# Performance work log

Hardware: AMD Instinct MI355X
Metric: run time of the kernel (lower is better)

## Reference

```python
import jax, jax.numpy as jnp
import numpy as np

NUM_USERS = 50000
NUM_ITEMS = 50000
N_NODES = NUM_USERS + NUM_ITEMS
DIM_FEAT = 256
HID = 128
EMB = 128
K = 3
N_EDGES = 1_600_000


def setup_inputs() -> dict:
    key = jax.random.key(0)
    ks = jax.random.split(key, 16)

    def xavier(k, shape):
        fan_in, fan_out = shape[-2], shape[-1]
        std = float(np.sqrt(2.0 / (fan_in + fan_out)))
        return jax.random.normal(k, shape, dtype=jnp.float32) * std

    return {
        "feat": jax.random.normal(ks[0], (NUM_ITEMS, DIM_FEAT), dtype=jnp.float32),
        "node_emb": jax.random.normal(ks[1], (N_NODES, EMB), dtype=jnp.float32),
        "src": jax.random.randint(ks[2], (N_EDGES,), 0, N_NODES, dtype=jnp.int32),
        "dst": jax.random.randint(ks[3], (N_EDGES,), 0, N_NODES, dtype=jnp.int32),
        "user_feat_emb": xavier(ks[4], (NUM_USERS, HID)),
        "trans_w": xavier(ks[5], (DIM_FEAT, HID)),
        "trans_b": jnp.zeros((HID,), dtype=jnp.float32),
        # layer 0: hidden->hidden; layers 1,2: emb->emb. hidden==emb so stack.
        "ws": xavier(ks[6], (K, HID, HID)),
        "des_w": xavier(ks[7], (K, HID, EMB)),
        "des_b": jnp.zeros((K, EMB), dtype=jnp.float32),
        # concat=True: outs[i] takes [h | u] of width hidden+emb
        "out_w": xavier(ks[8], (K, HID + EMB, EMB)),
        "out_b": jnp.zeros((K, EMB), dtype=jnp.float32),
    }


def reference(feat, node_emb, src, dst, user_feat_emb,
              trans_w, trans_b, ws, des_w, des_b, out_w, out_b):
    # feat = trans(feat); concat user embeddings; L2-normalize rows
    x = feat @ trans_w + trans_b                      # [num_items, HID]
    x = jnp.concatenate([user_feat_emb, x], axis=0)   # [N, HID]
    norm = jnp.linalg.norm(x, axis=1, keepdims=True)
    x = x / jnp.maximum(norm, 1e-12)

    lrelu = jax.nn.leaky_relu  # slope 0.01, matches F.leaky_relu default
    for i in range(K):
        # g.func(x, W): sparse adjacency aggregation (sum over in-edges) then dense W
        agg = jax.ops.segment_sum(x[src], dst, num_segments=N_NODES)  # [N, HID]
        h = lrelu(agg @ ws[i])                                        # [N, HID]
        u = lrelu(h @ des_w[i] + des_b[i] + node_emb)                 # [N, EMB]
        x = lrelu(jnp.concatenate([h, u], axis=1) @ out_w[i] + out_b[i])
    return x, user_feat_emb
```

## Files before the change

kernel.cpp:

```cpp
#include <hip/hip_runtime.h>

#define NN 100000
#define NU 50000
#define NI 50000
#define NE 1600000
#define NSLICE 2
#define SLICEW 50000

#define HSLICE 4
#define HCHUNK 64
#define HSW 25600
#define HEPC (NE/HCHUNK)

#define PREP_TW 14
#define PREP_CONV 6250
#define PREP_NORM 12500

typedef unsigned short u16;
typedef unsigned int u32;

typedef __attribute__((ext_vector_type(8))) short s16x8;
typedef __attribute__((ext_vector_type(4))) float f32x4;
typedef __attribute__((ext_vector_type(4))) unsigned short us4;

__device__ __forceinline__ float bf2f(u16 u){
  union { u32 i; float f; } v; v.i = ((u32)u) << 16; return v.f;
}
__device__ __forceinline__ u16 f2bf(float f){
  union { float f; u32 i; } v; v.f = f;
  u32 u = v.i;
  return (u16)((u + 0x7FFFu + ((u >> 16) & 1u)) >> 16);
}
__device__ __forceinline__ u32 pack2(float lo, float hi){
  return (u32)f2bf(lo) | ((u32)f2bf(hi) << 16);
}
__device__ __forceinline__ float lrelu(float x){ return x > 0.f ? x : 0.01f * x; }
__device__ __forceinline__ float san(float v){
  union { float f; u32 i; } u; u.f = v;
  return ((u.i & 0x7F800000u) == 0x7F800000u) ? 0.f : v;
}

__global__ __launch_bounds__(256) void prep(
    const float* __restrict__ trans_w, const float* __restrict__ wsw,
    const float* __restrict__ desw, const float* __restrict__ outw,
    u16* __restrict__ Ttw, u16* __restrict__ Tw, u16* __restrict__ Td, u16* __restrict__ To,
    const float* __restrict__ nemb, u16* __restrict__ nembB,
    const float* __restrict__ ufe, u16* __restrict__ X)
{
  __shared__ u16 L[128][136];
  int b = blockIdx.x, t = threadIdx.x;

  if (b < PREP_TW){
    const float* src; u16* dst; int stride;
    if (b < 2)      { src = trans_w + b*16384;        dst = Ttw + b*128;          stride = 256; }
    else if (b < 5) { int i = b-2; src = wsw  + i*16384; dst = Tw + i*16384;      stride = 128; }
    else if (b < 8) { int i = b-5; src = desw + i*16384; dst = Td + i*16384;      stride = 128; }
    else            { int i = (b-8)>>1, h = (b-8)&1;
                      src = outw + i*32768 + h*16384;    dst = To + i*32768 + h*128; stride = 256; }
    #pragma unroll
    for (int p = 0; p < 8; p++){
      int fi = (p*256 + t)*8;
      int r = fi >> 7, c = fi & 127;
      f32x4 v0 = *(const f32x4*)(src + r*128 + c);
      f32x4 v1 = *(const f32x4*)(src + r*128 + c + 4);
      L[c+0][r] = f2bf(san(v0.x)); L[c+1][r] = f2bf(san(v0.y));
      L[c+2][r] = f2bf(san(v0.z)); L[c+3][r] = f2bf(san(v0.w));
      L[c+4][r] = f2bf(san(v1.x)); L[c+5][r] = f2bf(san(v1.y));
      L[c+6][r] = f2bf(san(v1.z)); L[c+7][r] = f2bf(san(v1.w));
    }
    __syncthreads();
    #pragma unroll
    for (int p = 0; p < 8; p++){
      int fi = (p*256 + t)*8;
      int n = fi >> 7, k = fi & 127;
      us4 o0, o1;
      o0.x = L[n][k+0]; o0.y = L[n][k+1]; o0.z = L[n][k+2]; o0.w = L[n][k+3];
      o1.x = L[n][k+4]; o1.y = L[n][k+5]; o1.z = L[n][k+6]; o1.w = L[n][k+7];
      *(us4*)(dst + (size_t)n*stride + k)     = o0;
      *(us4*)(dst + (size_t)n*stride + k + 4) = o1;
    }
  } else if (b < PREP_TW + PREP_CONV){
    int i = (b - PREP_TW)*256 + t;
    size_t off = (size_t)i * 8;
    f32x4 v0 = *(const f32x4*)(nemb + off);
    f32x4 v1 = *(const f32x4*)(nemb + off + 4);
    us4 o0, o1;
    o0.x = f2bf(san(v0.x)); o0.y = f2bf(san(v0.y)); o0.z = f2bf(san(v0.z)); o0.w = f2bf(san(v0.w));
    o1.x = f2bf(san(v1.x)); o1.y = f2bf(san(v1.y)); o1.z = f2bf(san(v1.z)); o1.w = f2bf(san(v1.w));
    *(us4*)(nembB + off)     = o0;
    *(us4*)(nembB + off + 4) = o1;
  } else {
    int gid = (b - PREP_TW - PREP_CONV)*256 + t;
    int row = gid >> 6, lane = gid & 63;
    float2 v = *(const float2*)(ufe + (size_t)row*128 + lane*2);
    float a = san(v.x), bb = san(v.y);
    float ss = a*a + bb*bb;
    #pragma unroll
    for (int off = 32; off; off >>= 1) ss += __shfl_xor(ss, off, 64);
    float inv = 1.0f / fmaxf(sqrtf(ss), 1e-12f);
    *(u32*)(X + (size_t)row*128 + lane*2) = pack2(a*inv, bb*inv);
  }
}

__global__ __launch_bounds__(256, 4) void trans_items(
    const float* __restrict__ feat, const u16* __restrict__ Ttw,
    const float* __restrict__ tb, u16* __restrict__ X)
{
  __shared__ u16 Af[64][136];
  __shared__ float rowss[64][8];
  __shared__ float rnorm[64];

  int t = threadIdx.x;
  int r0 = blockIdx.x * 64;
  int w = t >> 6, lane = t & 63;
  int l15 = lane & 15, q = lane >> 4;
  int m0 = (w & 1) * 64, n0 = (w >> 1) * 32;

  f32x4 acc[4][2];
  #pragma unroll
  for (int mi = 0; mi < 4; mi++)
    #pragma unroll
    for (int ni = 0; ni < 2; ni++){ acc[mi][ni].x = 0.f; acc[mi][ni].y = 0.f; acc[mi][ni].z = 0.f; acc[mi][ni].w = 0.f; }

  for (int half = 0; half < 2; half++){
    __syncthreads();
    #pragma unroll
    for (int p = 0; p < 4; p++){
      int fi = (p*256 + t)*8;
      int r = fi >> 7, c = fi & 127;
      int row = r0 + r;
      us4 o0 = {0,0,0,0}, o1 = {0,0,0,0};
      if (row < NI){
        f32x4 v0 = *(const f32x4*)(feat + (size_t)row*256 + half*128 + c);
        f32x4 v1 = *(const f32x4*)(feat + (size_t)row*256 + half*128 + c + 4);
        o0.x = f2bf(san(v0.x)); o0.y = f2bf(san(v0.y)); o0.z = f2bf(san(v0.z)); o0.w = f2bf(san(v0.w));
        o1.x = f2bf(san(v1.x)); o1.y = f2bf(san(v1.y)); o1.z = f2bf(san(v1.z)); o1.w = f2bf(san(v1.w));
      }
      *(us4*)&Af[r][c]     = o0;
      *(us4*)&Af[r][c + 4] = o1;
    }
    __syncthreads();
    #pragma unroll
    for (int kc = 0; kc < 128; kc += 32){
      s16x8 afr[4], bfr[2];
      #pragma unroll
      for (int mi = 0; mi < 4; mi++)
        afr[mi] = *(const s16x8*)(Ttw + (size_t)(m0 + 16*mi + l15)*256 + half*128 + kc + 8*q);
      #pragma unroll
      for (int ni = 0; ni < 2; ni++) bfr[ni] = *(const s16x8*)&Af[n0 + 16*ni + l15][kc + 8*q];
      #pragma unroll
      for (int mi = 0; mi < 4; mi++)
        #pragma unroll
        for (int ni = 0; ni < 2; ni++)
          acc[mi][ni] = __builtin_amdgcn_mfma_f32_16x16x32_bf16(afr[mi], bfr[ni], acc[mi][ni], 0, 0, 0);
    }
  }

  float bias[4][4];
  #pragma unroll
  for (int mi = 0; mi < 4; mi++){
    int c0 = m0 + 16*mi + 4*q;
    f32x4 bv = *(const f32x4*)(tb + c0);
    bias[mi][0] = san(bv.x); bias[mi][1] = san(bv.y); bias[mi][2] = san(bv.z); bias[mi][3] = san(bv.w);
  }
  #pragma unroll
  for (int ni = 0; ni < 2; ni++){
    float ss = 0.f;
    #pragma unroll
    for (int mi = 0; mi < 4; mi++){
      float v0 = acc[mi][ni].x + bias[mi][0];
      float v1 = acc[mi][ni].y + bias[mi][1];
      float v2 = acc[mi][ni].z + bias[mi][2];
      float v3 = acc[mi][ni].w + bias[mi][3];
      ss += v0*v0 + v1*v1 + v2*v2 + v3*v3;
    }
    rowss[n0 + 16*ni + l15][(w & 1)*4 + q] = ss;
  }
  __syncthreads();
  if (t < 64){
    float s = 0.f;
    #pragma unroll
    for (int j = 0; j < 8; j++) s += rowss[t][j];
    rnorm[t] = 1.0f / fmaxf(sqrtf(s), 1e-12f);
  }
  __syncthreads();
  #pragma unroll
  for (int mi = 0; mi < 4; mi++){
    int c0 = m0 + 16*mi + 4*q;
    #pragma unroll
    for (int ni = 0; ni < 2; ni++){
      int r = n0 + 16*ni + l15;
      int row = r0 + r;
      if (row < NI){
        float inv = rnorm[r];
        us4 o;
        o.x = f2bf((acc[mi][ni].x + bias[mi][0]) * inv);
        o.y = f2bf((acc[mi][ni].y + bias[mi][1]) * inv);
        o.z = f2bf((acc[mi][ni].z + bias[mi][2]) * inv);
        o.w = f2bf((acc[mi][ni].w + bias[mi][3]) * inv);
        *(us4*)(X + (size_t)(NU + row)*128 + c0) = o;
      }
    }
  }
}

__global__ __launch_bounds__(1024) void hist_lds(
    const int* __restrict__ dst, u32* __restrict__ countsC)
{
  __shared__ u32 cnt[HSW];
  int b = blockIdx.x;
  int s = b / HCHUNK, c = b % HCHUNK;
  int t = threadIdx.x;
  for (int i = t; i < HSW; i += 1024) cnt[i] = 0;
  __syncthreads();
  int lo = s * HSW;
  int hi = min(lo + HSW, NN);
  int e0 = c * HEPC, e1 = e0 + HEPC;
  for (int e = e0 + t*4; e < e1; e += 4096){
    int4 d4 = *(const int4*)(dst + e);
    int d0 = min(max(d4.x, 0), NN-1);
    int d1 = min(max(d4.y, 0), NN-1);
    int d2 = min(max(d4.z, 0), NN-1);
    int d3 = min(max(d4.w, 0), NN-1);
    if (d0 >= lo && d0 < hi) atomicAdd(&cnt[d0 - lo], 1u);
    if (d1 >= lo && d1 < hi) atomicAdd(&cnt[d1 - lo], 1u);
    if (d2 >= lo && d2 < hi) atomicAdd(&cnt[d2 - lo], 1u);
    if (d3 >= lo && d3 < hi) atomicAdd(&cnt[d3 - lo], 1u);
  }
  __syncthreads();
  u32* outp = countsC + (size_t)c*NN + lo;
  int w = hi - lo;
  for (int i = t; i < w; i += 1024) outp[i] = cnt[i];
}

__global__ __launch_bounds__(256) void reduce_counts(
    const u32* __restrict__ countsC, int* __restrict__ counts)
{
  int v = blockIdx.x*256 + threadIdx.x;
  if (v < NN){
    u32 sum = 0;
    #pragma unroll
    for (int c = 0; c < HCHUNK; c++) sum += countsC[(size_t)c*NN + v];
    counts[v] = (int)sum;
  }
}

__global__ __launch_bounds__(1024) void scan_p1(
    const int* __restrict__ counts, int* __restrict__ row_ptr, int* __restrict__ bsum)
{
  __shared__ int wsum[16];
  __shared__ int woff[16];
  int t = threadIdx.x;
  int lane = t & 63, wid = t >> 6;
  int idx = blockIdx.x*4096 + t*4;
  int4 v = {0,0,0,0};
  if (idx < NN) v = *(const int4*)(counts + idx);
  int s4 = v.x + v.y + v.z + v.w;
  int s = s4;
  #pragma unroll
  for (int off = 1; off < 64; off <<= 1){
    int u = __shfl_up(s, off, 64);
    if (lane >= off) s += u;
  }
  if (lane == 63) wsum[wid] = s;
  __syncthreads();
  if (t < 16){
    int ws = wsum[t];
    int wscan = ws;
    #pragma unroll
    for (int off = 1; off < 16; off <<= 1){
      int u = __shfl_up(wscan, off, 64);
      if (t >= off) wscan += u;
    }
    woff[t] = wscan - ws;
    if (t == 15) bsum[blockIdx.x] = wscan;
  }
  __syncthreads();
  if (idx < NN){
    int e0 = woff[wid] + (s - s4);
    int4 o;
    o.x = e0; o.y = e0 + v.x; o.z = o.y + v.y; o.w = o.z + v.z;
    *(int4*)(row_ptr + idx) = o;
  }
}

__global__ __launch_bounds__(64) void scan_p2(int* __restrict__ bsum, int nb)
{
  int t = threadIdx.x;
  int v = (t < nb) ? bsum[t] : 0;
  int s = v;
  #pragma unroll
  for (int off = 1; off < 64; off <<= 1){
    int u = __shfl_up(s, off, 64);
    if (t >= off) s += u;
  }
  if (t < nb) bsum[t] = s - v;
}

__global__ __launch_bounds__(1024) void scan_p3(
    int* __restrict__ row_ptr, const int* __restrict__ bsum)
{
  int c = bsum[blockIdx.x];
  if (c == 0) return;
  int idx = blockIdx.x*4096 + threadIdx.x*4;
  if (idx < NN){
    int4 o = *(int4*)(row_ptr + idx);
    o.x += c; o.y += c; o.z += c; o.w += c;
    *(int4*)(row_ptr + idx) = o;
  }
}

__global__ __launch_bounds__(256) void fill_slice(
    const int* __restrict__ src, const int* __restrict__ dst,
    int* __restrict__ row_ptr, int* __restrict__ esrc, int d0, int d1)
{
  int e = blockIdx.x*256 + threadIdx.x;
  if (e < NE){
    int d = dst[e];
    if (d >= d0 && d < d1){
      d = min(max(d, 0), NN - 1);
      int pos = atomicAdd(&row_ptr[d], 1);
      pos = min(max(pos, 0), NE - 1);
      esrc[pos] = src[e];
    }
  }
}

#define ACC8(P) \
  a0 += bf2f((u16)(P.x & 0xFFFF)); a1 += bf2f((u16)(P.x >> 16)); \
  a2 += bf2f((u16)(P.y & 0xFFFF)); a3 += bf2f((u16)(P.y >> 16)); \
  a4 += bf2f((u16)(P.z & 0xFFFF)); a5 += bf2f((u16)(P.z >> 16)); \
  a6 += bf2f((u16)(P.w & 0xFFFF)); a7 += bf2f((u16)(P.w >> 16));

__global__ __launch_bounds__(256) void aggregate(
    const u16* __restrict__ X, const int* __restrict__ row_ptr,
    const int* __restrict__ esrc, u16* __restrict__ AGG)
{
  int gid = blockIdx.x*256 + threadIdx.x;
  int v = gid >> 6, lane = gid & 63;
  int sub = lane >> 4, li = lane & 15;
  int jb = (v == 0) ? 0 : row_ptr[v - 1];
  int je = row_ptr[v];
  jb = min(max(jb, 0), NE);
  je = min(max(je, jb), NE);

  float a0=0.f,a1=0.f,a2=0.f,a3=0.f,a4=0.f,a5=0.f,a6=0.f,a7=0.f;

  int j = jb + sub;
  for (; j + 12 < je; j += 16){
    int s0 = esrc[j];      s0 = min(max(s0, 0), NN - 1);
    int s1 = esrc[j + 4];  s1 = min(max(s1, 0), NN - 1);
    int s2 = esrc[j + 8];  s2 = min(max(s2, 0), NN - 1);
    int s3 = esrc[j + 12]; s3 = min(max(s3, 0), NN - 1);
    uint4 p0 = *(const uint4*)(X + (size_t)s0*128 + li*8);
    uint4 p1 = *(const uint4*)(X + (size_t)s1*128 + li*8);
    uint4 p2 = *(const uint4*)(X + (size_t)s2*128 + li*8);
    uint4 p3 = *(const uint4*)(X + (size_t)s3*128 + li*8);
    ACC8(p0); ACC8(p1); ACC8(p2); ACC8(p3);
  }
  for (; j + 4 < je; j += 8){
    int s0 = esrc[j];     s0 = min(max(s0, 0), NN - 1);
    int s1 = esrc[j + 4]; s1 = min(max(s1, 0), NN - 1);
    uint4 p0 = *(const uint4*)(X + (size_t)s0*128 + li*8);
    uint4 p1 = *(const uint4*)(X + (size_t)s1*128 + li*8);
    ACC8(p0); ACC8(p1);
  }
  for (; j < je; j += 4){
    int s0 = esrc[j]; s0 = min(max(s0, 0), NN - 1);
    uint4 p0 = *(const uint4*)(X + (size_t)s0*128 + li*8);
    ACC8(p0);
  }

  a0 += __shfl_xor(a0, 16, 64); a0 += __shfl_xor(a0, 32, 64);
  a1 += __shfl_xor(a1, 16, 64); a1 += __shfl_xor(a1, 32, 64);
  a2 += __shfl_xor(a2, 16, 64); a2 += __shfl_xor(a2, 32, 64);
  a3 += __shfl_xor(a3, 16, 64); a3 += __shfl_xor(a3, 32, 64);
  a4 += __shfl_xor(a4, 16, 64); a4 += __shfl_xor(a4, 32, 64);
  a5 += __shfl_xor(a5, 16, 64); a5 += __shfl_xor(a5, 32, 64);
  a6 += __shfl_xor(a6, 16, 64); a6 += __shfl_xor(a6, 32, 64);
  a7 += __shfl_xor(a7, 16, 64); a7 += __shfl_xor(a7, 32, 64);

  if (sub == 0){
    uint4 o;
    o.x = pack2(a0, a1); o.y = pack2(a2, a3);
    o.z = pack2(a4, a5); o.w = pack2(a6, a7);
    *(uint4*)(AGG + (size_t)v*128 + li*8) = o;
  }
}

__global__ __launch_bounds__(256, 2) void layer_fused(
    const u16* __restrict__ AGG, const u16* __restrict__ nembB,
    const u16* __restrict__ Twi, const u16* __restrict__ Tdi,
    const float* __restrict__ dbF, const u16* __restrict__ Toi,
    const float* __restrict__ obF, u16* __restrict__ XoutB,
    float* __restrict__ XoutF, int last)
{
  __shared__ __align__(16) u16 Ab[128][136];
  __shared__ __align__(16) u16 Hb[128][136];

  int t = threadIdx.x;
  int r0 = blockIdx.x * 128;
  int w = t >> 6, lane = t & 63;
  int l15 = lane & 15, q = lane >> 4;
  int m0 = (w & 1) * 64, n0 = (w >> 1) * 64;

  f32x4 acc[4][4];

#define ZERO_ACC() \
  { _Pragma("unroll") for (int mi = 0; mi < 4; mi++) \
      { _Pragma("unroll") for (int ni = 0; ni < 4; ni++) \
        { acc[mi][ni].x = 0.f; acc[mi][ni].y = 0.f; acc[mi][ni].z = 0.f; acc[mi][ni].w = 0.f; } } }

#define GEMMG(BARR, WBASE, WSTRIDE, WKOFF) \
  { s16x8 afr[4][4]; \
    _Pragma("unroll") for (int mi = 0; mi < 4; mi++) \
      { _Pragma("unroll") for (int kk = 0; kk < 4; kk++) \
          afr[mi][kk] = *(const s16x8*)((WBASE) + (size_t)(m0 + 16*mi + l15)*(WSTRIDE) + (WKOFF) + kk*32 + 8*q); } \
    _Pragma("unroll") for (int kk = 0; kk < 4; kk++){ \
      s16x8 bfr[4]; \
      _Pragma("unroll") for (int ni = 0; ni < 4; ni++) bfr[ni] = *(const s16x8*)&BARR[n0 + 16*ni + l15][kk*32 + 8*q]; \
      _Pragma("unroll") for (int mi = 0; mi < 4; mi++) \
        { _Pragma("unroll") for (int ni = 0; ni < 4; ni++) \
          acc[mi][ni] = __builtin_amdgcn_mfma_f32_16x16x32_bf16(afr[mi][kk], bfr[ni], acc[mi][ni], 0, 0, 0); } } }

  #pragma unroll
  for (int p = 0; p < 8; p++){
    int fi = (p*256 + t)*8;
    int r = fi >> 7, c = fi & 127;
    int row = r0 + r;
    us4 o0 = {0,0,0,0}, o1 = {0,0,0,0};
    if (row < NN){
      o0 = *(const us4*)(AGG + (size_t)row*128 + c);
      o1 = *(const us4*)(AGG + (size_t)row*128 + c + 4);
    }
    *(us4*)&Ab[r][c]     = o0;
    *(us4*)&Ab[r][c + 4] = o1;
  }
  __syncthreads();

  ZERO_ACC();
  GEMMG(Ab, Twi, 128, 0);

  #pragma unroll
  for (int mi = 0; mi < 4; mi++){
    #pragma unroll
    for (int ni = 0; ni < 4; ni++){
      us4 o;
      o.x = f2bf(lrelu(acc[mi][ni].x));
      o.y = f2bf(lrelu(acc[mi][ni].y));
      o.z = f2bf(lrelu(acc[mi][ni].z));
      o.w = f2bf(lrelu(acc[mi][ni].w));
      *(us4*)&Hb[n0 + 16*ni + l15][m0 + 16*mi + 4*q] = o;
    }
  }
  __syncthreads();

  ZERO_ACC();
  GEMMG(Hb, Tdi, 128, 0);

  #pragma unroll
  for (int mi = 0; mi < 4; mi++){
    int c0 = m0 + 16*mi + 4*q;
    f32x4 dbv = *(const f32x4*)(dbF + c0);
    float db0 = san(dbv.x), db1 = san(dbv.y), db2 = san(dbv.z), db3 = san(dbv.w);
    #pragma unroll
    for (int ni = 0; ni < 4; ni++){
      int r = n0 + 16*ni + l15;
      int row = r0 + r;
      float e0 = 0.f, e1 = 0.f, e2 = 0.f, e3 = 0.f;
      if (row < NN){
        us4 ne = *(const us4*)(nembB + (size_t)row*128 + c0);
        e0 = bf2f(ne.x); e1 = bf2f(ne.y); e2 = bf2f(ne.z); e3 = bf2f(ne.w);
      }
      us4 o;
      o.x = f2bf(lrelu(acc[mi][ni].x + db0 + e0));
      o.y = f2bf(lrelu(acc[mi][ni].y + db1 + e1));
      o.z = f2bf(lrelu(acc[mi][ni].z + db2 + e2));
      o.w = f2bf(lrelu(acc[mi][ni].w + db3 + e3));
      *(us4*)&Ab[r][c0] = o;
    }
  }
  __syncthreads();

  ZERO_ACC();
  GEMMG(Hb, Toi, 256, 0);
  GEMMG(Ab, Toi, 256, 128);

  #pragma unroll
  for (int mi = 0; mi < 4; mi++){
    int c0 = m0 + 16*mi + 4*q;
    f32x4 obv = *(const f32x4*)(obF + c0);
    float b0 = san(obv.x), b1 = san(obv.y), b2 = san(obv.z), b3 = san(obv.w);
    #pragma unroll
    for (int ni = 0; ni < 4; ni++){
      int r = n0 + 16*ni + l15;
      int row = r0 + r;
      if (row < NN){
        if (last){
          f32x4 o;
          o.x = lrelu(acc[mi][ni].x + b0);
          o.y = lrelu(acc[mi][ni].y + b1);
          o.z = lrelu(acc[mi][ni].z + b2);
          o.w = lrelu(acc[mi][ni].w + b3);
          *(f32x4*)(XoutF + (size_t)row*128 + c0) = o;
        } else {
          us4 o;
          o.x = f2bf(lrelu(acc[mi][ni].x + b0));
          o.y = f2bf(lrelu(acc[mi][ni].y + b1));
          o.z = f2bf(lrelu(acc[mi][ni].z + b2));
          o.w = f2bf(lrelu(acc[mi][ni].w + b3));
          *(us4*)(XoutB + (size_t)row*128 + c0) = o;
        }
      }
    }
  }
#undef ZERO_ACC
#undef GEMMG
}

__global__ void copy_ufe(const float4* __restrict__ s, float4* __restrict__ d, int n){
  int i = blockIdx.x*256 + threadIdx.x;
  if (i < n){
    float4 v = s[i];
    v.x = san(v.x); v.y = san(v.y); v.z = san(v.z); v.w = san(v.w);
    d[i] = v;
  }
}

extern "C" void kernel_launch(void* const* d_in, const int* in_sizes, int n_in,
                              void* d_out, int out_size, void* d_ws, size_t ws_size,
                              hipStream_t stream)
{
  const float* feat = (const float*)d_in[0];
  const float* nemb = (const float*)d_in[1];
  const int*   src  = (const int*)d_in[2];
  const int*   dst  = (const int*)d_in[3];
  const float* ufe  = (const float*)d_in[4];
  const float* tw   = (const float*)d_in[5];
  const float* tb   = (const float*)d_in[6];
  const float* wsw  = (const float*)d_in[7];
  const float* desw = (const float*)d_in[8];
  const float* desb = (const float*)d_in[9];
  const float* outw = (const float*)d_in[10];
  const float* outb = (const float*)d_in[11];

  float* out  = (float*)d_out;
  float* outU = out + (size_t)NN*128;

  u16* X = (u16*)out;
  u16* nembB = (u16*)outU;

  char* p = (char*)d_ws;
  u16*   AGG = (u16*)p;    p += (size_t)NN*128*2;
  u16*   Ttw = (u16*)p;    p += (size_t)2*16384*2;
  u16*   Tw  = (u16*)p;    p += (size_t)3*16384*2;
  u16*   Td  = (u16*)p;    p += (size_t)3*16384*2;
  u16*   To  = (u16*)p;    p += (size_t)3*32768*2;
  int* row_ptr = (int*)p;  p += (size_t)100004*4;
  int* counts  = (int*)p;  p += (size_t)100000*4;
  int* bsum    = (int*)p;  p += (size_t)64*4;
  int* esrc    = (int*)p;  p += (size_t)NE*4;
  u32* countsC = (u32*)AGG;

  prep<<<PREP_TW + PREP_CONV + PREP_NORM, 256, 0, stream>>>(
      tw, wsw, desw, outw, Ttw, Tw, Td, To, nemb, nembB, ufe, X);
  trans_items<<<(NI + 63)/64, 256, 0, stream>>>(feat, Ttw, tb, X);

  hist_lds<<<HSLICE*HCHUNK, 1024, 0, stream>>>(dst, countsC);
  reduce_counts<<<(NN + 255)/256, 256, 0, stream>>>(countsC, counts);
  int nsb = (NN + 4095)/4096;
  scan_p1<<<nsb, 1024, 0, stream>>>(counts, row_ptr, bsum);
  scan_p2<<<1, 64, 0, stream>>>(bsum, nsb);
  scan_p3<<<nsb, 1024, 0, stream>>>(row_ptr, bsum);
  for (int s = 0; s < NSLICE; s++){
    fill_slice<<<(NE + 255)/256, 256, 0, stream>>>(src, dst, row_ptr, esrc,
        s*SLICEW, (s == NSLICE-1) ? NN : (s+1)*SLICEW);
  }

  for (int i = 0; i < 3; i++){
    aggregate<<<NN/4, 256, 0, stream>>>(X, row_ptr, esrc, AGG);
    layer_fused<<<(NN + 127)/128, 256, 0, stream>>>(AGG, nembB,
        Tw + (size_t)i*16384, Td + (size_t)i*16384, desb + (size_t)i*128,
        To + (size_t)i*32768, outb + (size_t)i*128, X, out, (i == 2) ? 1 : 0);
  }
  copy_ufe<<<(NU*128/4 + 255)/256, 256, 0, stream>>>((const float4*)ufe, (float4*)outU, NU*128/4);
}
```

Measured before the change: 693.2 us.

## Fuse count reduction into scan, drop scan_p2, enlarge trans_items tile

Removes the separate reduce_counts and scan_p2 kernels. The scan's first pass now sums the 64 per-chunk histograms directly, and scan_p3 computes its block offset serially from bsum. trans_items now handles 128 rows per block, which doubles its accumulators and its shared-memory tile. The aim is fewer launches and more reuse of weights per block. In exchange, scan_p1 runs on only 25 blocks, each doing heavy serial loads, and the larger trans_items tile raises register and LDS pressure and halves the grid.

```diff
diff --git a/kernel.cpp b/kernel.cpp
--- a/kernel.cpp
+++ b/kernel.cpp
@@ -106,26 +106,26 @@
     const float* __restrict__ feat, const u16* __restrict__ Ttw,
     const float* __restrict__ tb, u16* __restrict__ X)
 {
-  __shared__ u16 Af[64][136];
-  __shared__ float rowss[64][8];
-  __shared__ float rnorm[64];
+  __shared__ u16 Af[128][136];
+  __shared__ float rowss[128][9];
+  __shared__ float rnorm[128];
 
   int t = threadIdx.x;
-  int r0 = blockIdx.x * 64;
+  int r0 = blockIdx.x * 128;
   int w = t >> 6, lane = t & 63;
   int l15 = lane & 15, q = lane >> 4;
-  int m0 = (w & 1) * 64, n0 = (w >> 1) * 32;
-
-  f32x4 acc[4][2];
+  int m0 = (w & 1) * 64, n0 = (w >> 1) * 64;
+
+  f32x4 acc[4][4];
   #pragma unroll
   for (int mi = 0; mi < 4; mi++)
     #pragma unroll
-    for (int ni = 0; ni < 2; ni++){ acc[mi][ni].x = 0.f; acc[mi][ni].y = 0.f; acc[mi][ni].z = 0.f; acc[mi][ni].w = 0.f; }
+    for (int ni = 0; ni < 4; ni++){ acc[mi][ni].x = 0.f; acc[mi][ni].y = 0.f; acc[mi][ni].z = 0.f; acc[mi][ni].w = 0.f; }
 
   for (int half = 0; half < 2; half++){
     __syncthreads();
     #pragma unroll
-    for (int p = 0; p < 4; p++){
+    for (int p = 0; p < 8; p++){
       int fi = (p*256 + t)*8;
       int r = fi >> 7, c = fi & 127;
       int row = r0 + r;
@@ -142,16 +142,16 @@
     __syncthreads();
     #pragma unroll
     for (int kc = 0; kc < 128; kc += 32){
-      s16x8 afr[4], bfr[2];
+      s16x8 afr[4], bfr[4];
       #pragma unroll
       for (int mi = 0; mi < 4; mi++)
         afr[mi] = *(const s16x8*)(Ttw + (size_t)(m0 + 16*mi + l15)*256 + half*128 + kc + 8*q);
       #pragma unroll
-      for (int ni = 0; ni < 2; ni++) bfr[ni] = *(const s16x8*)&Af[n0 + 16*ni + l15][kc + 8*q];
+      for (int ni = 0; ni < 4; ni++) bfr[ni] = *(const s16x8*)&Af[n0 + 16*ni + l15][kc + 8*q];
       #pragma unroll
       for (int mi = 0; mi < 4; mi++)
         #pragma unroll
-        for (int ni = 0; ni < 2; ni++)
+        for (int ni = 0; ni < 4; ni++)
           acc[mi][ni] = __builtin_amdgcn_mfma_f32_16x16x32_bf16(afr[mi], bfr[ni], acc[mi][ni], 0, 0, 0);
     }
   }
@@ -164,7 +164,7 @@
     bias[mi][0] = san(bv.x); bias[mi][1] = san(bv.y); bias[mi][2] = san(bv.z); bias[mi][3] = san(bv.w);
   }
   #pragma unroll
-  for (int ni = 0; ni < 2; ni++){
+  for (int ni = 0; ni < 4; ni++){
     float ss = 0.f;
     #pragma unroll
     for (int mi = 0; mi < 4; mi++){
@@ -177,7 +177,7 @@
     rowss[n0 + 16*ni + l15][(w & 1)*4 + q] = ss;
   }
   __syncthreads();
-  if (t < 64){
+  if (t < 128){
     float s = 0.f;
     #pragma unroll
     for (int j = 0; j < 8; j++) s += rowss[t][j];
@@ -188,7 +188,7 @@
   for (int mi = 0; mi < 4; mi++){
     int c0 = m0 + 16*mi + 4*q;
     #pragma unroll
-    for (int ni = 0; ni < 2; ni++){
+    for (int ni = 0; ni < 4; ni++){
       int r = n0 + 16*ni + l15;
       int row = r0 + r;
       if (row < NI){
@@ -233,20 +233,8 @@
   for (int i = t; i < w; i += 1024) outp[i] = cnt[i];
 }
 
-__global__ __launch_bounds__(256) void reduce_counts(
-    const u32* __restrict__ countsC, int* __restrict__ counts)
-{
-  int v = blockIdx.x*256 + threadIdx.x;
-  if (v < NN){
-    u32 sum = 0;
-    #pragma unroll
-    for (int c = 0; c < HCHUNK; c++) sum += countsC[(size_t)c*NN + v];
-    counts[v] = (int)sum;
-  }
-}
-
 __global__ __launch_bounds__(1024) void scan_p1(
-    const int* __restrict__ counts, int* __restrict__ row_ptr, int* __restrict__ bsum)
+    const u32* __restrict__ countsC, int* __restrict__ row_ptr, int* __restrict__ bsum)
 {
   __shared__ int wsum[16];
   __shared__ int woff[16];
@@ -254,7 +242,12 @@
   int lane = t & 63, wid = t >> 6;
   int idx = blockIdx.x*4096 + t*4;
   int4 v = {0,0,0,0};
-  if (idx < NN) v = *(const int4*)(counts + idx);
+  if (idx < NN){
+    for (int c = 0; c < HCHUNK; c++){
+      int4 cv = *(const int4*)(countsC + (size_t)c*NN + idx);
+      v.x += cv.x; v.y += cv.y; v.z += cv.z; v.w += cv.w;
+    }
+  }
   int s4 = v.x + v.y + v.z + v.w;
   int s = s4;
   #pragma unroll
@@ -284,25 +277,15 @@
   }
 }
 
-__global__ __launch_bounds__(64) void scan_p2(int* __restrict__ bsum, int nb)
-{
-  int t = threadIdx.x;
-  int v = (t < nb) ? bsum[t] : 0;
-  int s = v;
-  #pragma unroll
-  for (int off = 1; off < 64; off <<= 1){
-    int u = __shfl_up(s, off, 64);
-    if (t >= off) s += u;
-  }
-  if (t < nb) bsum[t] = s - v;
-}
-
 __global__ __launch_bounds__(1024) void scan_p3(
     int* __restrict__ row_ptr, const int* __restrict__ bsum)
 {
-  int c = bsum[blockIdx.x];
+  int b = blockIdx.x;
+  if (b == 0) return;
+  int c = 0;
+  for (int j = 0; j < b; j++) c += bsum[j];
   if (c == 0) return;
-  int idx = blockIdx.x*4096 + threadIdx.x*4;
+  int idx = b*4096 + threadIdx.x*4;
   if (idx < NN){
     int4 o = *(int4*)(row_ptr + idx);
     o.x += c; o.y += c; o.z += c; o.w += c;
@@ -557,20 +540,17 @@
   u16*   Td  = (u16*)p;    p += (size_t)3*16384*2;
   u16*   To  = (u16*)p;    p += (size_t)3*32768*2;
   int* row_ptr = (int*)p;  p += (size_t)100004*4;
-  int* counts  = (int*)p;  p += (size_t)100000*4;
   int* bsum    = (int*)p;  p += (size_t)64*4;
   int* esrc    = (int*)p;  p += (size_t)NE*4;
   u32* countsC = (u32*)AGG;
 
   prep<<<PREP_TW + PREP_CONV + PREP_NORM, 256, 0, stream>>>(
       tw, wsw, desw, outw, Ttw, Tw, Td, To, nemb, nembB, ufe, X);
-  trans_items<<<(NI + 63)/64, 256, 0, stream>>>(feat, Ttw, tb, X);
+  trans_items<<<(NI + 127)/128, 256, 0, stream>>>(feat, Ttw, tb, X);
 
   hist_lds<<<HSLICE*HCHUNK, 1024, 0, stream>>>(dst, countsC);
-  reduce_counts<<<(NN + 255)/256, 256, 0, stream>>>(countsC, counts);
   int nsb = (NN + 4095)/4096;
-  scan_p1<<<nsb, 1024, 0, stream>>>(counts, row_ptr, bsum);
-  scan_p2<<<1, 64, 0, stream>>>(bsum, nsb);
+  scan_p1<<<nsb, 1024, 0, stream>>>(countsC, row_ptr, bsum);
   scan_p3<<<nsb, 1024, 0, stream>>>(row_ptr, bsum);
   for (int s = 0; s < NSLICE; s++){
     fill_slice<<<(NE + 255)/256, 256, 0, stream>>>(src, dst, row_ptr, esrc,
```

After: 706.8 us. Within noise of the previous version (+2.0%).
